# Kernel tuning notes

Measured on AMD Instinct MI355X. Metric: run time of the kernel, lower is better.

The kernel has to match this reference:

```python
import jax, jax.numpy as jnp
import numpy as np

N_HEADS = 16
D_MODEL = 1024
D_HEAD = 64
MAX_SEQ_LEN = 1024


def setup_inputs() -> dict:
    key = jax.random.key(0)
    ks = jax.random.split(key, 7)
    std = np.sqrt(2.0 / (D_MODEL + D_HEAD)).astype(np.float32)
    hd = N_HEADS * D_HEAD
    # Weights stored as (in, out) so projection is x @ W (torch Linear y = x W^T).
    Wq = jax.random.normal(ks[0], (D_MODEL, hd), jnp.float32) * std
    Wk = jax.random.normal(ks[1], (D_MODEL, hd), jnp.float32) * std
    Wv = jax.random.normal(ks[2], (D_MODEL, hd), jnp.float32) * std
    Wo = jax.random.normal(ks[3], (hd, D_MODEL), jnp.float32) * (1.0 / np.sqrt(hd))
    bo = jnp.zeros((D_MODEL,), jnp.float32)
    rel_pos_bias = jax.random.normal(ks[4], (N_HEADS, MAX_SEQ_LEN), jnp.float32) * 0.02
    x = jax.random.normal(ks[5], (4, 1024, D_MODEL), jnp.float32)
    return {"x": x, "Wq": Wq, "Wk": Wk, "Wv": Wv, "Wo": Wo, "bo": bo,
            "rel_pos_bias": rel_pos_bias}


def _pos_bias(rel_pos_bias, T):
    # bias[h, i, j] = rel_pos_bias[h, MAX_SEQ_LEN - 1 - (i - j)] for j <= i, else 0
    i = jnp.arange(T)[:, None]
    j = jnp.arange(T)[None, :]
    idx = jnp.clip(MAX_SEQ_LEN - 1 - (i - j), 0, MAX_SEQ_LEN - 1)
    bias = rel_pos_bias[:, idx]                      # [H, T, T]
    return jnp.where((j <= i)[None], bias, 0.0)


def reference(x, Wq, Wk, Wv, Wo, bo, rel_pos_bias):
    B, T, _ = x.shape
    H, dh = N_HEADS, D_HEAD
    q = (x @ Wq).reshape(B, T, H, dh).transpose(0, 2, 1, 3)  # [B,H,T,dh]
    k = (x @ Wk).reshape(B, T, H, dh).transpose(0, 2, 1, 3)
    v = (x @ Wv).reshape(B, T, H, dh).transpose(0, 2, 1, 3)
    logits = jnp.einsum('bhqd,bhkd->bhqk', q, k)
    i = jnp.arange(T)[:, None]
    j = jnp.arange(T)[None, :]
    causal = jnp.where(j > i, -jnp.inf, 0.0)                 # [T,T]
    logits = logits + causal[None, None] + _pos_bias(rel_pos_bias, T)[None]
    logits = logits / dh                                     # note: /d_head, not sqrt
    probs = jax.nn.softmax(logits, axis=-1)
    out = jnp.einsum('bhqk,bhkd->bhqd', probs, v)            # [B,H,T,dh]
    out = out.transpose(0, 2, 1, 3).reshape(B, T, H * dh)
    return out @ Wo + bo
```

## Files before the change

kernel.cpp:

```cpp
#include <hip/hip_runtime.h>
#include <math.h>

#define BATCH 4
#define SEQ   1024
#define DM    1024
#define NH    16
#define DH    64
#define BT    (BATCH*SEQ)

typedef _Float16 f16x8 __attribute__((ext_vector_type(8)));
typedef _Float16 f16x4 __attribute__((ext_vector_type(4)));
typedef float    f32x4 __attribute__((ext_vector_type(4)));

#define GLL16(ldsdst, gsrc) \
  __builtin_amdgcn_global_load_lds((const __attribute__((address_space(1))) void*)(gsrc), \
                                   (__attribute__((address_space(3))) void*)(ldsdst), 16, 0, 0)

__global__ __launch_bounds__(256) void cvt_x(const float* __restrict__ x,
                                             _Float16* __restrict__ xh, int nquads)
{
    int i = blockIdx.x * blockDim.x + threadIdx.x;
    for (; i < nquads; i += gridDim.x * blockDim.x) {
        float4 f = ((const float4*)x)[i];
        f16x4 h;
        h[0] = (_Float16)f.x; h[1] = (_Float16)f.y;
        h[2] = (_Float16)f.z; h[3] = (_Float16)f.w;
        ((f16x4*)xh)[i] = h;
    }
}

__global__ __launch_bounds__(256) void cvt_wT(
    const float* __restrict__ W0, const float* __restrict__ W1,
    const float* __restrict__ W2, const float* __restrict__ W3,
    _Float16* __restrict__ T0, _Float16* __restrict__ T1,
    _Float16* __restrict__ T2, _Float16* __restrict__ T3)
{
    __shared__ _Float16 tile[64][72];
    const int z = blockIdx.z;
    const float* W = (z == 0) ? W0 : (z == 1) ? W1 : (z == 2) ? W2 : W3;
    _Float16*    T = (z == 0) ? T0 : (z == 1) ? T1 : (z == 2) ? T2 : T3;
    const int n0 = blockIdx.x * 64;
    const int k0 = blockIdx.y * 64;
    const int tid = threadIdx.x;
#pragma unroll
    for (int p = 0; p < 4; ++p) {
        int r = (tid >> 4) + p * 16;
        int c = (tid & 15) * 4;
        float4 f = *(const float4*)&W[(size_t)(k0 + r) * DM + n0 + c];
        f16x4 h;
        h[0] = (_Float16)f.x; h[1] = (_Float16)f.y;
        h[2] = (_Float16)f.z; h[3] = (_Float16)f.w;
        *(f16x4*)&tile[r][c] = h;
    }
    __syncthreads();
#pragma unroll
    for (int p = 0; p < 2; ++p) {
        int nr = (tid >> 3) + p * 32;
        int kc = (tid & 7) * 8;
        f16x8 vv;
#pragma unroll
        for (int i = 0; i < 8; ++i) vv[i] = tile[kc + i][nr];
        *(f16x8*)&T[(size_t)(n0 + nr) * DM + k0 + kc] = vv;
    }
}

template<int MODE>
__global__ __launch_bounds__(256) void gemm_mfma(
    const _Float16* __restrict__ A,
    const _Float16* __restrict__ B0, const _Float16* __restrict__ B1,
    const _Float16* __restrict__ B2,
    void* __restrict__ o0, void* __restrict__ o1, void* __restrict__ o2,
    const float* __restrict__ bias)
{
    __shared__ _Float16 As[128 * 32];
    __shared__ _Float16 Bs[128 * 32];

    const int tid = threadIdx.x;
    const int w   = tid >> 6;
    const int ln  = tid & 63;
    const int l15 = ln & 15;
    const int lg  = ln >> 4;
    const int wr  = w >> 1;
    const int wc  = w & 1;
    const int which = MODE ? (blockIdx.x >> 3) : 0;
    const int nl  = (blockIdx.x & 7) * 128;
    const int m0  = blockIdx.y * 128;

    const _Float16* Bt = (which == 0) ? B0 : (which == 1 ? B1 : B2);

    const int srow = ln >> 2;
    const int scol = (ln & 3) * 8;
    const _Float16* ga = A  + (size_t)(m0 + w * 32 + srow) * DM + scol;
    const _Float16* gb = Bt + (size_t)(nl + w * 32 + srow) * DM + scol;
    _Float16* la0 = &As[(w * 32 +  0) * 32];
    _Float16* la1 = &As[(w * 32 + 16) * 32];
    _Float16* lb0 = &Bs[(w * 32 +  0) * 32];
    _Float16* lb1 = &Bs[(w * 32 + 16) * 32];

    f32x4 acc[4][4];
#pragma unroll
    for (int i = 0; i < 4; ++i)
#pragma unroll
        for (int j = 0; j < 4; ++j) acc[i][j] = (f32x4){0.f, 0.f, 0.f, 0.f};

    for (int k0 = 0; k0 < DM; k0 += 32) {
        GLL16(la0, ga + k0);
        GLL16(la1, ga + k0 + (size_t)16 * DM);
        GLL16(lb0, gb + k0);
        GLL16(lb1, gb + k0 + (size_t)16 * DM);
        __syncthreads();

        f16x8 af[4], bf[4];
#pragma unroll
        for (int i = 0; i < 4; ++i)
            af[i] = *(const f16x8*)&As[(wr * 64 + i * 16 + l15) * 32 + lg * 8];
#pragma unroll
        for (int j = 0; j < 4; ++j)
            bf[j] = *(const f16x8*)&Bs[(wc * 64 + j * 16 + l15) * 32 + lg * 8];
#pragma unroll
        for (int i = 0; i < 4; ++i)
#pragma unroll
            for (int j = 0; j < 4; ++j)
                acc[i][j] = __builtin_amdgcn_mfma_f32_16x16x32_f16(af[i], bf[j], acc[i][j], 0, 0, 0);
        __syncthreads();
    }

    if (MODE == 1) {
        _Float16* outp = (which == 0) ? (_Float16*)o0
                        : (which == 1) ? (_Float16*)o1 : (_Float16*)o2;
        const float scale = (which == 0) ? 0.015625f : 1.0f;
#pragma unroll
        for (int i = 0; i < 4; ++i)
#pragma unroll
            for (int j = 0; j < 4; ++j) {
                int n  = nl + wc * 64 + j * 16 + l15;
                int hh = n >> 6, d = n & 63;
#pragma unroll
                for (int r = 0; r < 4; ++r) {
                    int m  = m0 + wr * 64 + i * 16 + lg * 4 + r;
                    int b_ = m >> 10, t_ = m & 1023;
                    outp[(((size_t)(b_ * NH + hh)) * SEQ + t_) * DH + d] =
                        (_Float16)(acc[i][j][r] * scale);
                }
            }
    } else {
        float* outp = (float*)o0;
#pragma unroll
        for (int i = 0; i < 4; ++i)
#pragma unroll
            for (int j = 0; j < 4; ++j) {
                int n = nl + wc * 64 + j * 16 + l15;
                float bz = bias[n];
#pragma unroll
                for (int r = 0; r < 4; ++r) {
                    int m = m0 + wr * 64 + i * 16 + lg * 4 + r;
                    outp[(size_t)m * DM + n] = acc[i][j][r] + bz;
                }
            }
    }
}

__global__ __launch_bounds__(256) void vtranspose(const _Float16* __restrict__ V,
                                                  _Float16* __restrict__ Vt)
{
    __shared__ _Float16 tile[64][72];
    const int bh = blockIdx.y;
    const int t0 = blockIdx.x * 64;
    const int tid = threadIdx.x;
    const int r = tid >> 3;
    const int c = (tid & 7) * 8;
    const size_t base = (size_t)bh * (SEQ * DH);
#pragma unroll
    for (int p = 0; p < 2; ++p) {
        int row = r + p * 32;
        *(f16x8*)&tile[row][c] = *(const f16x8*)&V[base + (size_t)(t0 + row) * DH + c];
    }
    __syncthreads();
#pragma unroll
    for (int p = 0; p < 2; ++p) {
        int d = r + p * 32;
        f16x8 vv;
#pragma unroll
        for (int i = 0; i < 8; ++i) vv[i] = tile[c + i][d];
        *(f16x8*)&Vt[base + (size_t)d * SEQ + t0 + c] = vv;
    }
}

__global__ __launch_bounds__(512) void attn_mfma(
    const _Float16* __restrict__ Q,
    const _Float16* __restrict__ K,
    const _Float16* __restrict__ Vt,
    const float* __restrict__ rpb,
    _Float16* __restrict__ ao)
{
    const int qt  = 15 - blockIdx.x;
    const int bh  = blockIdx.y;
    const int b_  = bh >> 4;
    const int h_  = bh & 15;
    const int tid = threadIdx.x;
    const int w   = tid >> 6;
    const int job = w >> 1;
    const int s   = w & 1;
    const int ln  = tid & 63;
    const int l15 = ln & 15;
    const int lg  = ln >> 4;

    __shared__ _Float16 Pb[8][16][72];
    __shared__ float mls[4][64][8];
    __shared__ float rpb_s[SEQ];

    *(float2*)&rpb_s[tid * 2] = *(const float2*)&rpb[h_ * SEQ + tid * 2];
    __syncthreads();

    const size_t qkb = (size_t)bh * (SEQ * DH);
    const int qr0 = qt * 64 + job * 16;

    f16x8 qa0, qa1;
    {
        const _Float16* qp = Q + qkb + (size_t)(qr0 + l15) * DH + lg * 8;
        qa0 = *(const f16x8*)qp;
        qa1 = *(const f16x8*)(qp + 32);
    }
    f32x4 acc[4];
    float mrow[4], lrow[4];
#pragma unroll
    for (int t = 0; t < 4; ++t) {
        acc[t] = (f32x4){0.f, 0.f, 0.f, 0.f};
        mrow[t] = -INFINITY;
        lrow[t] = 0.f;
    }
    const int ibase = qr0 + lg * 4;

#pragma unroll 1
    for (int kt = s; kt <= qt; kt += 2) {
        const _Float16* kp = K + qkb + (size_t)(kt * 64 + l15) * DH + lg * 8;
        f32x4 sv[4];
#pragma unroll
        for (int st = 0; st < 4; ++st) {
            f16x8 kb0 = *(const f16x8*)(kp + st * 16 * DH);
            f16x8 kb1 = *(const f16x8*)(kp + st * 16 * DH + 32);
            f32x4 z = (f32x4){0.f, 0.f, 0.f, 0.f};
            z = __builtin_amdgcn_mfma_f32_16x16x32_f16(qa0, kb0, z, 0, 0, 0);
            z = __builtin_amdgcn_mfma_f32_16x16x32_f16(qa1, kb1, z, 0, 0, 0);
            sv[st] = z;
        }
        const int bidx = 1023 - ibase + l15 + kt * 64;
        float tm[4] = {-INFINITY, -INFINITY, -INFINITY, -INFINITY};
#pragma unroll
        for (int st = 0; st < 4; ++st)
#pragma unroll
            for (int r = 0; r < 4; ++r) {
                int idx = bidx + st * 16 - r;
                float bv = rpb_s[idx <= 1023 ? idx : 1023];
                float val = (idx <= 1023) ? fmaf(bv, 0.015625f, sv[st][r]) : -INFINITY;
                sv[st][r] = val;
                tm[r] = fmaxf(tm[r], val);
            }
#pragma unroll
        for (int r = 0; r < 4; ++r) {
            tm[r] = fmaxf(tm[r], __shfl_xor(tm[r], 1, 16));
            tm[r] = fmaxf(tm[r], __shfl_xor(tm[r], 2, 16));
            tm[r] = fmaxf(tm[r], __shfl_xor(tm[r], 4, 16));
            tm[r] = fmaxf(tm[r], __shfl_xor(tm[r], 8, 16));
        }
        float corr[4], psum[4];
#pragma unroll
        for (int r = 0; r < 4; ++r) {
            float mn = fmaxf(mrow[r], tm[r]);
            corr[r]  = __expf(mrow[r] - mn);
            mrow[r]  = mn;
            psum[r]  = 0.f;
        }
#pragma unroll
        for (int st = 0; st < 4; ++st)
#pragma unroll
            for (int r = 0; r < 4; ++r) {
                float p = __expf(sv[st][r] - mrow[r]);
                sv[st][r] = p;
                psum[r] += p;
            }
#pragma unroll
        for (int r = 0; r < 4; ++r) {
            psum[r] += __shfl_xor(psum[r], 1, 16);
            psum[r] += __shfl_xor(psum[r], 2, 16);
            psum[r] += __shfl_xor(psum[r], 4, 16);
            psum[r] += __shfl_xor(psum[r], 8, 16);
            lrow[r] = lrow[r] * corr[r] + psum[r];
        }
#pragma unroll
        for (int t = 0; t < 4; ++t) {
            acc[t][0] *= corr[0]; acc[t][1] *= corr[1];
            acc[t][2] *= corr[2]; acc[t][3] *= corr[3];
        }
#pragma unroll
        for (int st = 0; st < 4; ++st)
#pragma unroll
            for (int r = 0; r < 4; ++r)
                Pb[w][lg * 4 + r][st * 16 + l15] = (_Float16)sv[st][r];
        f16x8 pa0 = *(const f16x8*)&Pb[w][l15][lg * 8];
        f16x8 pa1 = *(const f16x8*)&Pb[w][l15][32 + lg * 8];
        const _Float16* vp = Vt + qkb + (size_t)l15 * SEQ + kt * 64 + lg * 8;
#pragma unroll
        for (int dt = 0; dt < 4; ++dt) {
            f16x8 vb0 = *(const f16x8*)(vp + dt * 16 * SEQ);
            f16x8 vb1 = *(const f16x8*)(vp + dt * 16 * SEQ + 32);
            acc[dt] = __builtin_amdgcn_mfma_f32_16x16x32_f16(pa0, vb0, acc[dt], 0, 0, 0);
            acc[dt] = __builtin_amdgcn_mfma_f32_16x16x32_f16(pa1, vb1, acc[dt], 0, 0, 0);
        }
    }

    if (s == 1) {
        _Float16* mb = &Pb[w][0][0];
#pragma unroll
        for (int dt = 0; dt < 4; ++dt)
#pragma unroll
            for (int r = 0; r < 4; ++r)
                mb[ln * 16 + dt * 4 + r] = (_Float16)acc[dt][r];
#pragma unroll
        for (int r = 0; r < 4; ++r) {
            mls[job][ln][r]     = mrow[r];
            mls[job][ln][4 + r] = lrow[r];
        }
    }
    __syncthreads();
    if (s == 0) {
        const _Float16* mb = &Pb[w + 1][0][0];
        float c0[4], c1[4];
#pragma unroll
        for (int r = 0; r < 4; ++r) {
            float m1 = mls[job][ln][r];
            float l1 = mls[job][ln][4 + r];
            float mm = fmaxf(mrow[r], m1);
            c0[r] = __expf(mrow[r] - mm);
            c1[r] = __expf(m1 - mm);
            lrow[r] = lrow[r] * c0[r] + l1 * c1[r];
        }
        _Float16* aop = ao + ((size_t)b_ * SEQ + ibase) * DM + h_ * DH + l15;
#pragma unroll
        for (int r = 0; r < 4; ++r) {
            float inv = 1.f / lrow[r];
#pragma unroll
            for (int dt = 0; dt < 4; ++dt) {
                float v = acc[dt][r] * c0[r] + (float)mb[ln * 16 + dt * 4 + r] * c1[r];
                aop[(size_t)r * DM + dt * 16] = (_Float16)(v * inv);
            }
        }
    }
}

extern "C" void kernel_launch(void* const* d_in, const int* in_sizes, int n_in,
                              void* d_out, int out_size, void* d_ws, size_t ws_size,
                              hipStream_t stream)
{
    (void)in_sizes; (void)n_in; (void)out_size; (void)ws_size;
    const float* x   = (const float*)d_in[0];
    const float* Wq  = (const float*)d_in[1];
    const float* Wk  = (const float*)d_in[2];
    const float* Wv  = (const float*)d_in[3];
    const float* Wo  = (const float*)d_in[4];
    const float* bo  = (const float*)d_in[5];
    const float* rpb = (const float*)d_in[6];
    float* out = (float*)d_out;

    char* ws = (char*)d_ws;
    _Float16* xh  = (_Float16*)(ws);
    _Float16* q   = (_Float16*)(ws + (8u  << 20));
    _Float16* k   = (_Float16*)(ws + (16u << 20));
    _Float16* v   = (_Float16*)(ws + (24u << 20));
    _Float16* vt  = (_Float16*)(ws + (32u << 20));
    _Float16* aoh = (_Float16*)(ws + (40u << 20));
    _Float16* wqt = (_Float16*)(ws + (48u << 20));
    _Float16* wkt = (_Float16*)(ws + (50u << 20));
    _Float16* wvt = (_Float16*)(ws + (52u << 20));
    _Float16* wot = (_Float16*)(ws + (54u << 20));

    cvt_x<<<2048, 256, 0, stream>>>(x, xh, BT * DM / 4);
    cvt_wT<<<dim3(16, 16, 4), 256, 0, stream>>>(Wq, Wk, Wv, Wo, wqt, wkt, wvt, wot);
    gemm_mfma<1><<<dim3(24, 32), 256, 0, stream>>>(xh, wqt, wkt, wvt, q, k, v, nullptr);
    vtranspose<<<dim3(SEQ / 64, BATCH * NH), 256, 0, stream>>>(v, vt);
    attn_mfma<<<dim3(16, BATCH * NH), 512, 0, stream>>>(q, k, vt, rpb, aoh);
    gemm_mfma<0><<<dim3(8, 32), 256, 0, stream>>>(aoh, wot, nullptr, nullptr, out, nullptr, nullptr, bo);
}
```

Before: 267.6 us.

## Pair complementary causal query tiles per attention block for load balance

Each attention block now handles two query tiles, pr and 15-pr, one after the other, so every block does the same amount of causal work. The grid halves from 16 to 8 blocks per batch-head. Partial outputs and softmax statistics for both tiles go into a larger shared-memory buffer and are merged in one final pass after a single barrier. The cost is fewer blocks in flight, more shared memory per block (which can lower occupancy), and partials stored as fp16 before the merge.

```diff
diff --git a/kernel.cpp b/kernel.cpp
--- a/kernel.cpp
+++ b/kernel.cpp
@@ -193,158 +193,170 @@
     const float* __restrict__ rpb,
     _Float16* __restrict__ ao)
 {
-    const int qt  = 15 - blockIdx.x;
+    const int pr  = blockIdx.x;
     const int bh  = blockIdx.y;
     const int b_  = bh >> 4;
     const int h_  = bh & 15;
     const int tid = threadIdx.x;
     const int w   = tid >> 6;
-    const int job = w >> 1;
+    const int j   = w >> 1;
     const int s   = w & 1;
     const int ln  = tid & 63;
     const int l15 = ln & 15;
     const int lg  = ln >> 4;
 
     __shared__ _Float16 Pb[8][16][72];
-    __shared__ float mls[4][64][8];
-    __shared__ float rpb_s[SEQ];
+    __shared__ _Float16 part[8][2][1024];
+    __shared__ float    mlb[8][2][16][2];
+    __shared__ float    rpb_s[SEQ];
 
     *(float2*)&rpb_s[tid * 2] = *(const float2*)&rpb[h_ * SEQ + tid * 2];
     __syncthreads();
 
     const size_t qkb = (size_t)bh * (SEQ * DH);
-    const int qr0 = qt * 64 + job * 16;
-
-    f16x8 qa0, qa1;
+
+#pragma unroll 1
+    for (int ji = 0; ji < 2; ++ji) {
+        const int qt  = ji ? (15 - pr) : pr;
+        const int qr0 = qt * 64 + j * 16;
+        const int ibase = qr0 + lg * 4;
+
+        f16x8 qa0, qa1;
+        {
+            const _Float16* qp = Q + qkb + (size_t)(qr0 + l15) * DH + lg * 8;
+            qa0 = *(const f16x8*)qp;
+            qa1 = *(const f16x8*)(qp + 32);
+        }
+        f32x4 acc[4];
+        float mrow[4], lrow[4];
+#pragma unroll
+        for (int t = 0; t < 4; ++t) {
+            acc[t] = (f32x4){0.f, 0.f, 0.f, 0.f};
+            mrow[t] = -INFINITY;
+            lrow[t] = 0.f;
+        }
+
+#pragma unroll 1
+        for (int kt = s; kt <= qt; kt += 2) {
+            const _Float16* kp = K + qkb + (size_t)(kt * 64 + l15) * DH + lg * 8;
+            f32x4 sv[4];
+#pragma unroll
+            for (int st = 0; st < 4; ++st) {
+                f16x8 kb0 = *(const f16x8*)(kp + st * 16 * DH);
+                f16x8 kb1 = *(const f16x8*)(kp + st * 16 * DH + 32);
+                f32x4 z = (f32x4){0.f, 0.f, 0.f, 0.f};
+                z = __builtin_amdgcn_mfma_f32_16x16x32_f16(qa0, kb0, z, 0, 0, 0);
+                z = __builtin_amdgcn_mfma_f32_16x16x32_f16(qa1, kb1, z, 0, 0, 0);
+                sv[st] = z;
+            }
+            const int bidx = 1023 - ibase + l15 + kt * 64;
+            float tm[4] = {-INFINITY, -INFINITY, -INFINITY, -INFINITY};
+#pragma unroll
+            for (int st = 0; st < 4; ++st)
+#pragma unroll
+                for (int r = 0; r < 4; ++r) {
+                    int idx = bidx + st * 16 - r;
+                    float bv = rpb_s[idx <= 1023 ? idx : 1023];
+                    float val = (idx <= 1023) ? fmaf(bv, 0.015625f, sv[st][r]) : -INFINITY;
+                    sv[st][r] = val;
+                    tm[r] = fmaxf(tm[r], val);
+                }
+#pragma unroll
+            for (int r = 0; r < 4; ++r) {
+                tm[r] = fmaxf(tm[r], __shfl_xor(tm[r], 1, 16));
+                tm[r] = fmaxf(tm[r], __shfl_xor(tm[r], 2, 16));
+                tm[r] = fmaxf(tm[r], __shfl_xor(tm[r], 4, 16));
+                tm[r] = fmaxf(tm[r], __shfl_xor(tm[r], 8, 16));
+            }
+            float corr[4], psum[4];
+#pragma unroll
+            for (int r = 0; r < 4; ++r) {
+                float mn = fmaxf(mrow[r], tm[r]);
+                corr[r]  = __expf(mrow[r] - mn);
+                mrow[r]  = mn;
+                psum[r]  = 0.f;
+            }
+#pragma unroll
+            for (int st = 0; st < 4; ++st)
+#pragma unroll
+                for (int r = 0; r < 4; ++r) {
+                    float p = __expf(sv[st][r] - mrow[r]);
+                    sv[st][r] = p;
+                    psum[r] += p;
+                }
+#pragma unroll
+            for (int r = 0; r < 4; ++r) {
+                psum[r] += __shfl_xor(psum[r], 1, 16);
+                psum[r] += __shfl_xor(psum[r], 2, 16);
+                psum[r] += __shfl_xor(psum[r], 4, 16);
+                psum[r] += __shfl_xor(psum[r], 8, 16);
+                lrow[r] = lrow[r] * corr[r] + psum[r];
+            }
+#pragma unroll
+            for (int t = 0; t < 4; ++t) {
+                acc[t][0] *= corr[0]; acc[t][1] *= corr[1];
+                acc[t][2] *= corr[2]; acc[t][3] *= corr[3];
+            }
+#pragma unroll
+            for (int st = 0; st < 4; ++st)
+#pragma unroll
+                for (int r = 0; r < 4; ++r)
+                    Pb[w][lg * 4 + r][st * 16 + l15] = (_Float16)sv[st][r];
+            f16x8 pa0 = *(const f16x8*)&Pb[w][l15][lg * 8];
+            f16x8 pa1 = *(const f16x8*)&Pb[w][l15][32 + lg * 8];
+            const _Float16* vp = Vt + qkb + (size_t)l15 * SEQ + kt * 64 + lg * 8;
+#pragma unroll
+            for (int dt = 0; dt < 4; ++dt) {
+                f16x8 vb0 = *(const f16x8*)(vp + dt * 16 * SEQ);
+                f16x8 vb1 = *(const f16x8*)(vp + dt * 16 * SEQ + 32);
+                acc[dt] = __builtin_amdgcn_mfma_f32_16x16x32_f16(pa0, vb0, acc[dt], 0, 0, 0);
+                acc[dt] = __builtin_amdgcn_mfma_f32_16x16x32_f16(pa1, vb1, acc[dt], 0, 0, 0);
+            }
+        }
+
+#pragma unroll
+        for (int dt = 0; dt < 4; ++dt)
+#pragma unroll
+            for (int r = 0; r < 4; ++r)
+                part[w][ji][ln * 16 + dt * 4 + r] = (_Float16)acc[dt][r];
+        if (l15 == 0) {
+#pragma unroll
+            for (int r = 0; r < 4; ++r) {
+                mlb[w][ji][lg * 4 + r][0] = mrow[r];
+                mlb[w][ji][lg * 4 + r][1] = lrow[r];
+            }
+        }
+    }
+    __syncthreads();
+
     {
-        const _Float16* qp = Q + qkb + (size_t)(qr0 + l15) * DH + lg * 8;
-        qa0 = *(const f16x8*)qp;
-        qa1 = *(const f16x8*)(qp + 32);
-    }
-    f32x4 acc[4];
-    float mrow[4], lrow[4];
-#pragma unroll
-    for (int t = 0; t < 4; ++t) {
-        acc[t] = (f32x4){0.f, 0.f, 0.f, 0.f};
-        mrow[t] = -INFINITY;
-        lrow[t] = 0.f;
-    }
-    const int ibase = qr0 + lg * 4;
-
-#pragma unroll 1
-    for (int kt = s; kt <= qt; kt += 2) {
-        const _Float16* kp = K + qkb + (size_t)(kt * 64 + l15) * DH + lg * 8;
-        f32x4 sv[4];
-#pragma unroll
-        for (int st = 0; st < 4; ++st) {
-            f16x8 kb0 = *(const f16x8*)(kp + st * 16 * DH);
-            f16x8 kb1 = *(const f16x8*)(kp + st * 16 * DH + 32);
-            f32x4 z = (f32x4){0.f, 0.f, 0.f, 0.f};
-            z = __builtin_amdgcn_mfma_f32_16x16x32_f16(qa0, kb0, z, 0, 0, 0);
-            z = __builtin_amdgcn_mfma_f32_16x16x32_f16(qa1, kb1, z, 0, 0, 0);
-            sv[st] = z;
-        }
-        const int bidx = 1023 - ibase + l15 + kt * 64;
-        float tm[4] = {-INFINITY, -INFINITY, -INFINITY, -INFINITY};
-#pragma unroll
-        for (int st = 0; st < 4; ++st)
-#pragma unroll
-            for (int r = 0; r < 4; ++r) {
-                int idx = bidx + st * 16 - r;
-                float bv = rpb_s[idx <= 1023 ? idx : 1023];
-                float val = (idx <= 1023) ? fmaf(bv, 0.015625f, sv[st][r]) : -INFINITY;
-                sv[st][r] = val;
-                tm[r] = fmaxf(tm[r], val);
-            }
+        const int qs  = w & 1;
+        const int j2  = w >> 1;
+        const int qt2 = qs ? (15 - pr) : pr;
+        const int wA  = j2 * 2;
+        const int wB  = wA + 1;
+        const int ibase2 = qt2 * 64 + j2 * 16 + lg * 4;
+        float c0[4], c1[4], linv[4];
 #pragma unroll
         for (int r = 0; r < 4; ++r) {
-            tm[r] = fmaxf(tm[r], __shfl_xor(tm[r], 1, 16));
-            tm[r] = fmaxf(tm[r], __shfl_xor(tm[r], 2, 16));
-            tm[r] = fmaxf(tm[r], __shfl_xor(tm[r], 4, 16));
-            tm[r] = fmaxf(tm[r], __shfl_xor(tm[r], 8, 16));
-        }
-        float corr[4], psum[4];
-#pragma unroll
-        for (int r = 0; r < 4; ++r) {
-            float mn = fmaxf(mrow[r], tm[r]);
-            corr[r]  = __expf(mrow[r] - mn);
-            mrow[r]  = mn;
-            psum[r]  = 0.f;
-        }
-#pragma unroll
-        for (int st = 0; st < 4; ++st)
-#pragma unroll
-            for (int r = 0; r < 4; ++r) {
-                float p = __expf(sv[st][r] - mrow[r]);
-                sv[st][r] = p;
-                psum[r] += p;
-            }
-#pragma unroll
-        for (int r = 0; r < 4; ++r) {
-            psum[r] += __shfl_xor(psum[r], 1, 16);
-            psum[r] += __shfl_xor(psum[r], 2, 16);
-            psum[r] += __shfl_xor(psum[r], 4, 16);
-            psum[r] += __shfl_xor(psum[r], 8, 16);
-            lrow[r] = lrow[r] * corr[r] + psum[r];
-        }
-#pragma unroll
-        for (int t = 0; t < 4; ++t) {
-            acc[t][0] *= corr[0]; acc[t][1] *= corr[1];
-            acc[t][2] *= corr[2]; acc[t][3] *= corr[3];
-        }
-#pragma unroll
-        for (int st = 0; st < 4; ++st)
-#pragma unroll
-            for (int r = 0; r < 4; ++r)
-                Pb[w][lg * 4 + r][st * 16 + l15] = (_Float16)sv[st][r];
-        f16x8 pa0 = *(const f16x8*)&Pb[w][l15][lg * 8];
-        f16x8 pa1 = *(const f16x8*)&Pb[w][l15][32 + lg * 8];
-        const _Float16* vp = Vt + qkb + (size_t)l15 * SEQ + kt * 64 + lg * 8;
-#pragma unroll
-        for (int dt = 0; dt < 4; ++dt) {
-            f16x8 vb0 = *(const f16x8*)(vp + dt * 16 * SEQ);
-            f16x8 vb1 = *(const f16x8*)(vp + dt * 16 * SEQ + 32);
-            acc[dt] = __builtin_amdgcn_mfma_f32_16x16x32_f16(pa0, vb0, acc[dt], 0, 0, 0);
-            acc[dt] = __builtin_amdgcn_mfma_f32_16x16x32_f16(pa1, vb1, acc[dt], 0, 0, 0);
-        }
-    }
-
-    if (s == 1) {
-        _Float16* mb = &Pb[w][0][0];
-#pragma unroll
-        for (int dt = 0; dt < 4; ++dt)
-#pragma unroll
-            for (int r = 0; r < 4; ++r)
-                mb[ln * 16 + dt * 4 + r] = (_Float16)acc[dt][r];
-#pragma unroll
-        for (int r = 0; r < 4; ++r) {
-            mls[job][ln][r]     = mrow[r];
-            mls[job][ln][4 + r] = lrow[r];
-        }
-    }
-    __syncthreads();
-    if (s == 0) {
-        const _Float16* mb = &Pb[w + 1][0][0];
-        float c0[4], c1[4];
-#pragma unroll
-        for (int r = 0; r < 4; ++r) {
-            float m1 = mls[job][ln][r];
-            float l1 = mls[job][ln][4 + r];
-            float mm = fmaxf(mrow[r], m1);
-            c0[r] = __expf(mrow[r] - mm);
+            float m0 = mlb[wA][qs][lg * 4 + r][0];
+            float l0 = mlb[wA][qs][lg * 4 + r][1];
+            float m1 = mlb[wB][qs][lg * 4 + r][0];
+            float l1 = mlb[wB][qs][lg * 4 + r][1];
+            float mm = fmaxf(m0, m1);
+            c0[r] = __expf(m0 - mm);
             c1[r] = __expf(m1 - mm);
-            lrow[r] = lrow[r] * c0[r] + l1 * c1[r];
-        }
-        _Float16* aop = ao + ((size_t)b_ * SEQ + ibase) * DM + h_ * DH + l15;
-#pragma unroll
-        for (int r = 0; r < 4; ++r) {
-            float inv = 1.f / lrow[r];
+            linv[r] = 1.f / (l0 * c0[r] + l1 * c1[r]);
+        }
+        _Float16* aop = ao + ((size_t)b_ * SEQ + ibase2) * DM + h_ * DH + l15;
+#pragma unroll
+        for (int r = 0; r < 4; ++r)
 #pragma unroll
             for (int dt = 0; dt < 4; ++dt) {
-                float v = acc[dt][r] * c0[r] + (float)mb[ln * 16 + dt * 4 + r] * c1[r];
-                aop[(size_t)r * DM + dt * 16] = (_Float16)(v * inv);
-            }
-        }
+                float v = (float)part[wA][qs][ln * 16 + dt * 4 + r] * c0[r]
+                        + (float)part[wB][qs][ln * 16 + dt * 4 + r] * c1[r];
+                aop[(size_t)r * DM + dt * 16] = (_Float16)(v * linv[r]);
+            }
     }
 }
 
@@ -378,6 +390,6 @@
     cvt_wT<<<dim3(16, 16, 4), 256, 0, stream>>>(Wq, Wk, Wv, Wo, wqt, wkt, wvt, wot);
     gemm_mfma<1><<<dim3(24, 32), 256, 0, stream>>>(xh, wqt, wkt, wvt, q, k, v, nullptr);
     vtranspose<<<dim3(SEQ / 64, BATCH * NH), 256, 0, stream>>>(v, vt);
-    attn_mfma<<<dim3(16, BATCH * NH), 512, 0, stream>>>(q, k, vt, rpb, aoh);
+    attn_mfma<<<dim3(8, BATCH * NH), 512, 0, stream>>>(q, k, vt, rpb, aoh);
     gemm_mfma<0><<<dim3(8, 32), 256, 0, stream>>>(aoh, wot, nullptr, nullptr, out, nullptr, nullptr, bo);
 }
```

Result: faster. 228.7 us (-14.5%).
